# Kernel tuning notes

Measured on AMD Instinct MI355X. Metric: run time of the kernel, lower is better.

Reference implementation:

```python
import jax, jax.numpy as jnp
import numpy as np

WS = 11      # window_size
SIGMA = 1.5
C1 = 0.01 ** 2
C2 = 0.03 ** 2


def _window(channel):
    g = np.exp(-((np.arange(WS) - WS // 2) ** 2) / (2.0 * SIGMA ** 2))
    g = (g / g.sum()).astype(np.float32)
    w2 = np.outer(g, g)  # [WS, WS]
    return jnp.asarray(np.broadcast_to(w2, (channel, 1, WS, WS)).copy())


def _blur(x, w, channel):
    pad = WS // 2
    return jax.lax.conv_general_dilated(
        x, w, window_strides=(1, 1), padding=[(pad, pad), (pad, pad)],
        dimension_numbers=("NCHW", "OIHW", "NCHW"),
        feature_group_count=channel)


def _ssim(img1, img2, w, channel):
    mu1 = _blur(img1, w, channel)
    mu2 = _blur(img2, w, channel)
    mu1_sq = mu1 * mu1
    mu2_sq = mu2 * mu2
    mu1_mu2 = mu1 * mu2
    sigma1_sq = _blur(img1 * img1, w, channel) - mu1_sq
    sigma2_sq = _blur(img2 * img2, w, channel) - mu2_sq
    sigma12 = _blur(img1 * img2, w, channel) - mu1_mu2
    ssim_map = ((2.0 * mu1_mu2 + C1) * (2.0 * sigma12 + C2)) / (
        (mu1_sq + mu2_sq + C1) * (sigma1_sq + sigma2_sq + C2))
    return ssim_map.mean()  # size_average=True


def setup_inputs() -> dict:
    key = jax.random.key(0)
    k1, k2, k3 = jax.random.split(key, 3)
    B, C, H, W = 16, 3, 512, 512
    return {
        "fused_img": jax.random.uniform(k1, (B, C, H, W), dtype=jnp.float32),
        "source_img1": jax.random.uniform(k2, (B, C, H, W), dtype=jnp.float32),
        "source_img2": jax.random.uniform(k3, (B, C, H, W), dtype=jnp.float32),
    }


def reference(fused_img, source_img1, source_img2):
    channel = fused_img.shape[1]
    w = _window(channel).astype(fused_img.dtype)
    ssim1 = _ssim(fused_img, source_img1, w, channel)
    ssim2 = _ssim(fused_img, source_img2, w, channel)
    return 1.0 - (ssim1 + ssim2) / 2.0
```

## Files before the change

kernel.cpp:

```cpp
#include <hip/hip_runtime.h>
#include <hip/hip_fp16.h>
#include <cmath>

#define HALO 5
#define TSX 32
#define TILE_H 128
#define NSTEP 8
#define CH 16
#define RING 42
#define HSTR 36
#define PLANE (RING * HSTR)
#define WIDTH 512
#define HEIGHT 512

struct GW { float g[11]; };

__device__ __forceinline__ uint32_t pk2(float a, float b)
{
    auto h = __builtin_amdgcn_cvt_pkrtz(a, b);
    return __builtin_bit_cast(uint32_t, h);
}

__device__ __forceinline__ float ssim2(float mu1, float mu2,
                                       float x2b, float y2b, float xyb)
{
    const float C1 = 1e-4f, C2 = 9e-4f;
    float mu12 = mu1 * mu2;
    float num  = (2.f * mu12 + C1) * (2.f * (xyb - mu12) + C2);
    float den  = (mu1 * mu1 + mu2 * mu2 + C1) *
                 ((x2b - mu1 * mu1) + (y2b - mu2 * mu2) + C2);
    return num * __builtin_amdgcn_rcpf(den);
}

template<bool CX, bool CY>
__device__ __forceinline__ void hblur_row(
    const float* __restrict__ rowf, const float* __restrict__ rowa,
    const float* __restrict__ rowb, bool yok, int gx0, int slot, int qA,
    uint32_t (* __restrict__ hb)[PLANE], const GW& gw)
{
    float acc[4][8];
    #pragma unroll
    for (int jj = 0; jj < 4; ++jj)
        #pragma unroll
        for (int q = 0; q < 8; ++q) acc[jj][q] = 0.f;

    #pragma unroll
    for (int k = 0; k < 5; ++k) {
        const int g = gx0 + 4 * k;
        float4 vf, va, vb;
        if (CX || CY) {
            bool ok = true;
            if (CY) ok = yok;
            if (CX) ok = ok && ((unsigned)g <= (unsigned)(WIDTH - 4));
            vf = ok ? *(const float4*)(rowf + g) : make_float4(0,0,0,0);
            va = ok ? *(const float4*)(rowa + g) : make_float4(0,0,0,0);
            vb = ok ? *(const float4*)(rowb + g) : make_float4(0,0,0,0);
        } else {
            vf = *(const float4*)(rowf + g);
            va = *(const float4*)(rowa + g);
            vb = *(const float4*)(rowb + g);
        }
        const float fs[4] = { vf.x, vf.y, vf.z, vf.w };
        const float as[4] = { va.x, va.y, va.z, va.w };
        const float bs[4] = { vb.x, vb.y, vb.z, vb.w };
        #pragma unroll
        for (int cc = 0; cc < 4; ++cc) {
            const int tt = 4 * k + cc - 3;
            if (tt < 0 || tt > 13) continue;
            const float f = fs[cc], a = as[cc], b = bs[cc];
            float p[8];
            p[0] = f; p[1] = a; p[2] = b;
            p[3] = f * f; p[4] = a * a; p[5] = b * b;
            p[6] = f * a; p[7] = f * b;
            #pragma unroll
            for (int jj = 0; jj < 4; ++jj) {
                const int u = tt - jj;
                if (u >= 0 && u <= 10) {
                    const float w = gw.g[u];
                    #pragma unroll
                    for (int q = 0; q < 8; ++q)
                        acc[jj][q] = fmaf(w, p[q], acc[jj][q]);
                }
            }
        }
    }
    #pragma unroll
    for (int p = 0; p < 4; ++p) {
        uint4 v = make_uint4(pk2(acc[0][2*p], acc[0][2*p+1]),
                             pk2(acc[1][2*p], acc[1][2*p+1]),
                             pk2(acc[2][2*p], acc[2][2*p+1]),
                             pk2(acc[3][2*p], acc[3][2*p+1]));
        *(uint4*)(&hb[p][slot * HSTR + 4 * qA]) = v;
    }
}

template<bool CX, bool CY>
__device__ __forceinline__ float tile_compute(
    const float* __restrict__ fI, const float* __restrict__ aI,
    const float* __restrict__ bI, uint32_t (* __restrict__ hb)[PLANE],
    const GW& gw, int tid, int x0, int y0, size_t pbase)
{
    const int rA  = tid >> 3;
    const int qA  = tid & 7;
    const int gx0 = x0 + 4 * qA - 8;
    const int jB  = tid & 31;
    const int rgB = (tid >> 5) & 3;

    __half2 wh[11];
    #pragma unroll
    for (int i = 0; i < 11; ++i) wh[i] = __float2half2_rn(gw.g[i]);

    float part = 0.f;

    if (rA < 26) {
        const int yy = y0 - HALO + rA;
        const bool yok = CY ? ((unsigned)yy < (unsigned)HEIGHT) : true;
        hblur_row<CX, CY>(fI + pbase + (size_t)yy * WIDTH,
                          aI + pbase + (size_t)yy * WIDTH,
                          bI + pbase + (size_t)yy * WIDTH,
                          yok, gx0, rA, qA, hb, gw);
    }
    __syncthreads();

    #pragma unroll 1
    for (int s = 0; s < NSTEP; ++s) {
        if (tid < 128) {
            if (s < NSTEP - 1) {
                const int t = CH * s + RING - CH + rA;
                int slot = t;
                slot -= (slot >= RING) ? RING : 0;
                slot -= (slot >= RING) ? RING : 0;
                slot -= (slot >= RING) ? RING : 0;
                const int yy = y0 - HALO + t;
                const bool yok = CY ? ((unsigned)yy < (unsigned)HEIGHT) : true;
                hblur_row<CX, CY>(fI + pbase + (size_t)yy * WIDTH,
                                  aI + pbase + (size_t)yy * WIDTH,
                                  bI + pbase + (size_t)yy * WIDTH,
                                  yok, gx0, slot, qA, hb, gw);
            }
        } else {
            int sb = CH * s + 4 * rgB;
            sb -= (sb >= RING) ? RING : 0;
            sb -= (sb >= RING) ? RING : 0;
            __half2 acc2[4][4];
            #pragma unroll
            for (int ri = 0; ri < 4; ++ri)
                #pragma unroll
                for (int p = 0; p < 4; ++p)
                    acc2[ri][p] = __float2half2_rn(0.f);
            #pragma unroll
            for (int k = 0; k < 14; ++k) {
                int t = sb + k;
                t -= (t >= RING) ? RING : 0;
                const uint32_t* hp = &hb[0][t * HSTR + jB];
                __half2 hv[4];
                #pragma unroll
                for (int p = 0; p < 4; ++p)
                    hv[p] = __builtin_bit_cast(__half2, hp[p * PLANE]);
                #pragma unroll
                for (int ri = 0; ri < 4; ++ri) {
                    const int u = k - ri;
                    if (u >= 0 && u <= 10) {
                        #pragma unroll
                        for (int p = 0; p < 4; ++p)
                            acc2[ri][p] = __hfma2(wh[u], hv[p], acc2[ri][p]);
                    }
                }
            }
            #pragma unroll
            for (int ri = 0; ri < 4; ++ri) {
                const float F  = __low2float (acc2[ri][0]);
                const float A  = __high2float(acc2[ri][0]);
                const float B  = __low2float (acc2[ri][1]);
                const float F2 = __high2float(acc2[ri][1]);
                const float A2 = __low2float (acc2[ri][2]);
                const float B2 = __high2float(acc2[ri][2]);
                const float FA = __low2float (acc2[ri][3]);
                const float FB = __high2float(acc2[ri][3]);
                part += ssim2(F, A, F2, A2, FA);
                part += ssim2(F, B, F2, B2, FB);
            }
        }
        __syncthreads();
    }
    return part;
}

__global__ __launch_bounds__(256, 4)
void ssim_tile(const float* __restrict__ fI, const float* __restrict__ aI,
               const float* __restrict__ bI, float* __restrict__ bsum,
               GW gw)
{
    __shared__ __align__(16) uint32_t hb[4][PLANE];
    __shared__ float red[4];

    const int tid = threadIdx.x;
    const int x0 = blockIdx.x * TSX;
    const int y0 = blockIdx.y * TILE_H;
    const size_t pbase = (size_t)blockIdx.z * (size_t)(WIDTH * HEIGHT);

    const bool ex = (blockIdx.x == 0) || (blockIdx.x == gridDim.x - 1);
    const bool ey = (blockIdx.y == 0) || (blockIdx.y == gridDim.y - 1);

    float part;
    if (!ex && !ey)
        part = tile_compute<false, false>(fI, aI, bI, hb, gw, tid, x0, y0, pbase);
    else if (!ex)
        part = tile_compute<false, true >(fI, aI, bI, hb, gw, tid, x0, y0, pbase);
    else if (!ey)
        part = tile_compute<true,  false>(fI, aI, bI, hb, gw, tid, x0, y0, pbase);
    else
        part = tile_compute<true,  true >(fI, aI, bI, hb, gw, tid, x0, y0, pbase);

    #pragma unroll
    for (int off = 32; off > 0; off >>= 1) part += __shfl_down(part, off);
    if ((tid & 63) == 0) red[tid >> 6] = part;
    __syncthreads();
    if (tid == 0) {
        int bid = blockIdx.x + gridDim.x * (blockIdx.y + gridDim.y * blockIdx.z);
        bsum[bid] = red[0] + red[1] + red[2] + red[3];
    }
}

__global__ __launch_bounds__(256)
void ssim_final(const float* __restrict__ bsum, float* __restrict__ out,
                int nb, float invTwoN)
{
    __shared__ float sred[4];
    float s = 0.f;
    for (int i = threadIdx.x; i < nb; i += 256) s += bsum[i];
    #pragma unroll
    for (int off = 32; off > 0; off >>= 1) s += __shfl_down(s, off);
    if ((threadIdx.x & 63) == 0) sred[threadIdx.x >> 6] = s;
    __syncthreads();
    if (threadIdx.x == 0)
        out[0] = 1.f - (sred[0] + sred[1] + sred[2] + sred[3]) * invTwoN;
}

extern "C" void kernel_launch(void* const* d_in, const int* in_sizes, int n_in,
                              void* d_out, int out_size, void* d_ws, size_t ws_size,
                              hipStream_t stream)
{
    const float* f  = (const float*)d_in[0];
    const float* s1 = (const float*)d_in[1];
    const float* s2 = (const float*)d_in[2];
    float* out  = (float*)d_out;
    float* bsum = (float*)d_ws;

    const int N = in_sizes[0];
    const int planes = N / (WIDTH * HEIGHT);

    GW gw;
    double gd[11], gs = 0.0;
    for (int i = 0; i < 11; ++i) {
        double d = (double)(i - 5);
        gd[i] = exp(-(d * d) / 4.5);
        gs += gd[i];
    }
    for (int i = 0; i < 11; ++i) gw.g[i] = (float)(gd[i] / gs);

    dim3 grid(WIDTH / TSX, HEIGHT / TILE_H, planes);
    const int nb = (WIDTH / TSX) * (HEIGHT / TILE_H) * planes;
    ssim_tile<<<grid, dim3(256), 0, stream>>>(f, s1, s2, bsum, gw);
    ssim_final<<<1, dim3(256), 0, stream>>>(bsum, out, nb, 0.5f / (float)N);
}
```

Measured before the change: 264.2 us.

## Replace producer/consumer warp split with all-thread chunked horizontal then vertical phases

Drops the scheme where half the block did horizontal blur while the other half did the vertical pass. Every thread now computes horizontal rows, then every thread computes vertical blur and SSIM, over 4 chunks of 32 rows each. The half2 Gaussian weights are packed on the host and read from kernel arguments instead of being converted per thread. Occupancy hint lowered to 3 blocks per CU; the split loses overlap between the phases but uses all waves for each phase.

```diff
diff --git a/kernel.cpp b/kernel.cpp
--- a/kernel.cpp
+++ b/kernel.cpp
@@ -1,19 +1,20 @@
 #include <hip/hip_runtime.h>
 #include <hip/hip_fp16.h>
 #include <cmath>
+#include <cstring>
 
 #define HALO 5
 #define TSX 32
 #define TILE_H 128
-#define NSTEP 8
-#define CH 16
+#define NCHUNK 4
+#define CH 32
 #define RING 42
 #define HSTR 36
 #define PLANE (RING * HSTR)
 #define WIDTH 512
 #define HEIGHT 512
 
-struct GW { float g[11]; };
+struct GW { float g[11]; uint32_t wpk[11]; };
 
 __device__ __forceinline__ uint32_t pk2(float a, float b)
 {
@@ -104,15 +105,11 @@
     const int qA  = tid & 7;
     const int gx0 = x0 + 4 * qA - 8;
     const int jB  = tid & 31;
-    const int rgB = (tid >> 5) & 3;
-
-    __half2 wh[11];
-    #pragma unroll
-    for (int i = 0; i < 11; ++i) wh[i] = __float2half2_rn(gw.g[i]);
+    const int rgB = tid >> 5;
 
     float part = 0.f;
 
-    if (rA < 26) {
+    {
         const int yy = y0 - HALO + rA;
         const bool yok = CY ? ((unsigned)yy < (unsigned)HEIGHT) : true;
         hblur_row<CX, CY>(fI + pbase + (size_t)yy * WIDTH,
@@ -120,73 +117,82 @@
                           bI + pbase + (size_t)yy * WIDTH,
                           yok, gx0, rA, qA, hb, gw);
     }
+    if (rA < 10) {
+        const int t  = 32 + rA;
+        const int yy = y0 - HALO + t;
+        const bool yok = CY ? ((unsigned)yy < (unsigned)HEIGHT) : true;
+        hblur_row<CX, CY>(fI + pbase + (size_t)yy * WIDTH,
+                          aI + pbase + (size_t)yy * WIDTH,
+                          bI + pbase + (size_t)yy * WIDTH,
+                          yok, gx0, t, qA, hb, gw);
+    }
     __syncthreads();
 
     #pragma unroll 1
-    for (int s = 0; s < NSTEP; ++s) {
-        if (tid < 128) {
-            if (s < NSTEP - 1) {
-                const int t = CH * s + RING - CH + rA;
-                int slot = t;
-                slot -= (slot >= RING) ? RING : 0;
-                slot -= (slot >= RING) ? RING : 0;
-                slot -= (slot >= RING) ? RING : 0;
-                const int yy = y0 - HALO + t;
-                const bool yok = CY ? ((unsigned)yy < (unsigned)HEIGHT) : true;
-                hblur_row<CX, CY>(fI + pbase + (size_t)yy * WIDTH,
-                                  aI + pbase + (size_t)yy * WIDTH,
-                                  bI + pbase + (size_t)yy * WIDTH,
-                                  yok, gx0, slot, qA, hb, gw);
-            }
-        } else {
-            int sb = CH * s + 4 * rgB;
-            sb -= (sb >= RING) ? RING : 0;
-            sb -= (sb >= RING) ? RING : 0;
-            __half2 acc2[4][4];
-            #pragma unroll
-            for (int ri = 0; ri < 4; ++ri)
-                #pragma unroll
-                for (int p = 0; p < 4; ++p)
-                    acc2[ri][p] = __float2half2_rn(0.f);
-            #pragma unroll
-            for (int k = 0; k < 14; ++k) {
-                int t = sb + k;
-                t -= (t >= RING) ? RING : 0;
-                const uint32_t* hp = &hb[0][t * HSTR + jB];
-                __half2 hv[4];
-                #pragma unroll
-                for (int p = 0; p < 4; ++p)
-                    hv[p] = __builtin_bit_cast(__half2, hp[p * PLANE]);
-                #pragma unroll
-                for (int ri = 0; ri < 4; ++ri) {
-                    const int u = k - ri;
-                    if (u >= 0 && u <= 10) {
-                        #pragma unroll
-                        for (int p = 0; p < 4; ++p)
-                            acc2[ri][p] = __hfma2(wh[u], hv[p], acc2[ri][p]);
-                    }
+    for (int c = 0; c < NCHUNK; ++c) {
+        if (c) {
+            const int t = CH * c + 10 + rA;
+            int slot = t;
+            slot -= (slot >= RING) ? RING : 0;
+            slot -= (slot >= RING) ? RING : 0;
+            slot -= (slot >= RING) ? RING : 0;
+            const int yy = y0 - HALO + t;
+            const bool yok = CY ? ((unsigned)yy < (unsigned)HEIGHT) : true;
+            hblur_row<CX, CY>(fI + pbase + (size_t)yy * WIDTH,
+                              aI + pbase + (size_t)yy * WIDTH,
+                              bI + pbase + (size_t)yy * WIDTH,
+                              yok, gx0, slot, qA, hb, gw);
+            __syncthreads();
+        }
+
+        int sb = CH * c + 4 * rgB;
+        sb -= (sb >= RING) ? RING : 0;
+        sb -= (sb >= RING) ? RING : 0;
+        __half2 acc2[4][4];
+        #pragma unroll
+        for (int ri = 0; ri < 4; ++ri)
+            #pragma unroll
+            for (int p = 0; p < 4; ++p)
+                acc2[ri][p] = __float2half2_rn(0.f);
+        #pragma unroll
+        for (int k = 0; k < 14; ++k) {
+            int t = sb + k;
+            t -= (t >= RING) ? RING : 0;
+            const uint32_t* hp = &hb[0][t * HSTR + jB];
+            __half2 hv[4];
+            #pragma unroll
+            for (int p = 0; p < 4; ++p)
+                hv[p] = __builtin_bit_cast(__half2, hp[p * PLANE]);
+            #pragma unroll
+            for (int ri = 0; ri < 4; ++ri) {
+                const int u = k - ri;
+                if (u >= 0 && u <= 10) {
+                    const __half2 w = __builtin_bit_cast(__half2, gw.wpk[u]);
+                    #pragma unroll
+                    for (int p = 0; p < 4; ++p)
+                        acc2[ri][p] = __hfma2(w, hv[p], acc2[ri][p]);
                 }
             }
-            #pragma unroll
-            for (int ri = 0; ri < 4; ++ri) {
-                const float F  = __low2float (acc2[ri][0]);
-                const float A  = __high2float(acc2[ri][0]);
-                const float B  = __low2float (acc2[ri][1]);
-                const float F2 = __high2float(acc2[ri][1]);
-                const float A2 = __low2float (acc2[ri][2]);
-                const float B2 = __high2float(acc2[ri][2]);
-                const float FA = __low2float (acc2[ri][3]);
-                const float FB = __high2float(acc2[ri][3]);
-                part += ssim2(F, A, F2, A2, FA);
-                part += ssim2(F, B, F2, B2, FB);
-            }
+        }
+        #pragma unroll
+        for (int ri = 0; ri < 4; ++ri) {
+            const float F  = __low2float (acc2[ri][0]);
+            const float A  = __high2float(acc2[ri][0]);
+            const float B  = __low2float (acc2[ri][1]);
+            const float F2 = __high2float(acc2[ri][1]);
+            const float A2 = __low2float (acc2[ri][2]);
+            const float B2 = __high2float(acc2[ri][2]);
+            const float FA = __low2float (acc2[ri][3]);
+            const float FB = __high2float(acc2[ri][3]);
+            part += ssim2(F, A, F2, A2, FA);
+            part += ssim2(F, B, F2, B2, FB);
         }
         __syncthreads();
     }
     return part;
 }
 
-__global__ __launch_bounds__(256, 4)
+__global__ __launch_bounds__(256, 3)
 void ssim_tile(const float* __restrict__ fI, const float* __restrict__ aI,
                const float* __restrict__ bI, float* __restrict__ bsum,
                GW gw)
@@ -237,6 +243,18 @@
         out[0] = 1.f - (sred[0] + sred[1] + sred[2] + sred[3]) * invTwoN;
 }
 
+static uint16_t f2h(float f)
+{
+    uint32_t x; std::memcpy(&x, &f, 4);
+    uint32_t s = (x >> 16) & 0x8000u;
+    int      e = (int)((x >> 23) & 0xff) - 127 + 15;
+    uint32_t m = x & 0x007fffffu;
+    uint32_t base = ((uint32_t)e << 10) | (m >> 13);
+    uint32_t rem  = m & 0x1fffu;
+    if (rem > 0x1000u || (rem == 0x1000u && (base & 1u))) base++;
+    return (uint16_t)(s | base);
+}
+
 extern "C" void kernel_launch(void* const* d_in, const int* in_sizes, int n_in,
                               void* d_out, int out_size, void* d_ws, size_t ws_size,
                               hipStream_t stream)
@@ -257,7 +275,11 @@
         gd[i] = exp(-(d * d) / 4.5);
         gs += gd[i];
     }
-    for (int i = 0; i < 11; ++i) gw.g[i] = (float)(gd[i] / gs);
+    for (int i = 0; i < 11; ++i) {
+        gw.g[i] = (float)(gd[i] / gs);
+        uint32_t h = f2h(gw.g[i]);
+        gw.wpk[i] = (h << 16) | h;
+    }
 
     dim3 grid(WIDTH / TSX, HEIGHT / TILE_H, planes);
     const int nb = (WIDTH / TSX) * (HEIGHT / TILE_H) * planes;
```

Result: faster. 220.6 us (-16.5%).
